# Kernel optimization log

Measured on AMD Instinct MI355X. Metric: run time of the kernel, lower is better.

## Reference

```python
import jax, jax.numpy as jnp
import numpy as np

DIM = 2048
ORDER = 1
# upper-triangular index pairs (i<j), row-major over i then j — matches torch loop order
_IU_ROWS, _IU_COLS = np.triu_indices(DIM, k=1)


def setup_inputs() -> dict:
    key = jax.random.key(0)
    k1, k2 = jax.random.split(key)
    num_params = DIM * (DIM - 1) // 2
    x = jax.random.normal(k1, (4, 4096, DIM), dtype=jnp.float32)
    angles = jax.random.normal(k2, (num_params,), dtype=jnp.float32) * 0.01
    bias = jnp.zeros((DIM,), dtype=jnp.float32)
    return {"x": x, "angles": angles, "bias": bias}


def _skew_symmetric(angles):
    # A[i,j] = angles[k], A[j,i] = -angles[k] for upper-tri (i<j)
    A = jnp.zeros((DIM, DIM), dtype=angles.dtype)
    A = A.at[_IU_ROWS, _IU_COLS].set(angles)
    return A - A.T


def _cayley_approx(A, order=ORDER):
    # W = (I + A + ... + A^order) @ (I + A)
    I = jnp.eye(DIM, dtype=A.dtype)
    inv_approx = I
    A_power = A
    for _ in range(order):
        inv_approx = inv_approx + A_power
        A_power = A_power @ A
    return inv_approx @ (I + A)


def reference(x, angles, bias):
    A = _skew_symmetric(angles)
    W = _cayley_approx(A)
    # [b, s, d] @ [d, d] -> [b, s, d]
    out = jnp.einsum('bsd,de->bse', x, W) + bias
    return out
```

## Files before the change

### kernel.cpp

```cpp
#include <hip/hip_runtime.h>
#include <stdint.h>

#define DIM 2048

typedef short short8 __attribute__((ext_vector_type(8)));
typedef float f32x4 __attribute__((ext_vector_type(4)));

__device__ __forceinline__ unsigned short f2bf(float f) {
    union { float f; unsigned int u; } v;
    v.f = f;
    unsigned int r = v.u + 0x7FFFu + ((v.u >> 16) & 1u);
    return (unsigned short)(r >> 16);
}
__device__ __forceinline__ float bf2f(unsigned short u) {
    union { unsigned int u; float f; } v;
    v.u = ((unsigned int)u) << 16;
    return v.f;
}

__device__ __forceinline__ void async16(const unsigned short* g, unsigned short* l) {
    __builtin_amdgcn_global_load_lds(
        (__attribute__((address_space(1))) void*)(uintptr_t)g,
        (__attribute__((address_space(3))) void*)(uintptr_t)l,
        16, 0, 0);
}

__global__ __launch_bounds__(256) void build_A_tiled(const float* __restrict__ ang,
                                                     unsigned short* __restrict__ A) {
    __shared__ float tile[64][65];
    int b = blockIdx.x;
    int ti = 0, rem = b;
    while (rem >= 32 - ti) { rem -= 32 - ti; ++ti; }
    const int tj = ti + rem;
    const int t  = threadIdx.x;
    const int lj = t & 63;
    const int lw = t >> 6;
    const bool diag = (ti == tj);

#pragma unroll
    for (int m = 0; m < 16; ++m) {
        const int li = lw * 16 + m;
        const int i = ti * 64 + li;
        const int j = tj * 64 + lj;
        float v = 0.0f;
        if (i < j) v = ang[i * (4095 - i) / 2 + (j - i - 1)];
        tile[li][lj] = v;
    }
    __syncthreads();

#pragma unroll
    for (int m = 0; m < 16; ++m) {
        const int li = lw * 16 + m;
        float v;
        if (diag) {
            if (li < lj)      v =  tile[li][lj];
            else if (li > lj) v = -tile[lj][li];
            else              v = 0.0f;
        } else {
            v = tile[li][lj];
        }
        A[(size_t)(ti * 64 + li) * DIM + tj * 64 + lj] = f2bf(v);
    }
    if (!diag) {
#pragma unroll
        for (int m = 0; m < 16; ++m) {
            const int li = lw * 16 + m;
            A[(size_t)(tj * 64 + li) * DIM + ti * 64 + lj] = f2bf(-tile[lj][li]);
        }
    }
}

__global__ __launch_bounds__(256) void s64sym_cvt(
        const unsigned short* __restrict__ A,
        unsigned short* __restrict__ Wt,
        const float* __restrict__ x,
        unsigned short* __restrict__ xbf) {
    __shared__ __align__(16) unsigned short smem[12288];
    unsigned short* ldsA = smem;
    unsigned short* ldsB = smem + 4096;
    float* ldsT = (float*)smem;

    if (blockIdx.x >= 528) {
        const int i = ((blockIdx.x - 528) * 256 + threadIdx.x) * 8;
        const float4 v0 = *(const float4*)(x + i);
        const float4 v1 = *(const float4*)(x + i + 4);
        unsigned short o[8];
        o[0] = f2bf(v0.x); o[1] = f2bf(v0.y); o[2] = f2bf(v0.z); o[3] = f2bf(v0.w);
        o[4] = f2bf(v1.x); o[5] = f2bf(v1.y); o[6] = f2bf(v1.z); o[7] = f2bf(v1.w);
        *(short8*)(xbf + i) = *(short8*)(o);
        return;
    }

    const int K = DIM, N = DIM;
    const int t = threadIdx.x;
    const int swz = (blockIdx.x & 7) * 66 + (blockIdx.x >> 3);
    int ti = 0, rem = swz;
    while (rem >= 32 - ti) { rem -= 32 - ti; ++ti; }
    const int tj = ti + rem;
    const int bm = ti * 64;
    const int bn = tj * 64;

    const int lane = t & 63;
    const int wave = t >> 6;
    const int waveM = (wave >> 1) * 32;
    const int waveN = (wave & 1) * 32;
    const int fm = lane & 15;
    const int fq = lane >> 4;

    f32x4 acc[2][2];
#pragma unroll
    for (int i = 0; i < 2; ++i)
#pragma unroll
        for (int j = 0; j < 2; ++j)
            acc[i][j] = (f32x4){0.f, 0.f, 0.f, 0.f};

    const int trow   = t >> 3;
    const int tchunk = (t & 7) ^ (trow & 7);
    const unsigned short* gA = A + (size_t)(bm + trow) * K + tchunk * 8;
    const unsigned short* gB = A + (size_t)(bn + trow) * K + tchunk * 8;
    const size_t rowskip = (size_t)32 * K;
    unsigned short* lA = ldsA + t * 8;
    unsigned short* lB = ldsB + t * 8;

    for (int kt = 0; kt < K; kt += 64) {
        __syncthreads();
        async16(gA + kt, lA);
        async16(gA + kt + rowskip, lA + 2048);
        async16(gB + kt, lB);
        async16(gB + kt + rowskip, lB + 2048);
        __syncthreads();

#pragma unroll
        for (int ks = 0; ks < 2; ++ks) {
            short8 af[2], bfv[2];
#pragma unroll
            for (int i = 0; i < 2; ++i) {
                const int rowA = waveM + i * 16 + fm;
                const int rowB = waveN + i * 16 + fm;
                af[i]  = *(const short8*)(ldsA + rowA * 64 + (((ks << 2) + fq) ^ (rowA & 7)) * 8);
                bfv[i] = *(const short8*)(ldsB + rowB * 64 + (((ks << 2) + fq) ^ (rowB & 7)) * 8);
            }
#pragma unroll
            for (int i = 0; i < 2; ++i)
#pragma unroll
                for (int j = 0; j < 2; ++j)
                    acc[i][j] = __builtin_amdgcn_mfma_f32_16x16x32_bf16(
                        af[i], bfv[j], acc[i][j], 0, 0, 0);
        }
    }

    __syncthreads();
#pragma unroll
    for (int i = 0; i < 2; ++i) {
#pragma unroll
        for (int j = 0; j < 2; ++j) {
            const int lj = waveN + j * 16 + fm;
            const int gj = bn + lj;
#pragma unroll
            for (int r = 0; r < 4; ++r) {
                const int li = waveM + i * 16 + fq * 4 + r;
                const int gi = bm + li;
                const float a = bf2f(A[(size_t)gi * N + gj]);
                const float s = acc[i][j][r];
                const float d = (gi == gj) ? 1.0f : 0.0f;
                Wt[(size_t)gi * N + gj] = f2bf(d - 2.0f * a - s);
                ldsT[lj * 65 + li] = d + 2.0f * a - s;
            }
        }
    }
    __syncthreads();
    {
        const int r  = t >> 2;
        const int cb = (t & 3) * 16;
        unsigned short o[16];
#pragma unroll
        for (int u = 0; u < 16; ++u)
            o[u] = f2bf(ldsT[r * 65 + cb + u]);
        *(short8*)(Wt + (size_t)(bn + r) * N + bm + cb)     = *(short8*)(o);
        *(short8*)(Wt + (size_t)(bn + r) * N + bm + cb + 8) = *(short8*)(o + 8);
    }
}


#define WAITV(N) asm volatile("s_waitcnt vmcnt(" #N ")" ::: "memory")
#define BAR() do { asm volatile("" ::: "memory"); __builtin_amdgcn_s_barrier(); asm volatile("" ::: "memory"); } while (0)

#define STG_A(BUF, R0, KT) async16(gA + (size_t)(R0) * 2048 + (KT), &ldsA[BUF][(R0) * 64 + t * 8])
#define STG_B(BUF, R0, KT) async16(gB + (size_t)(R0) * 2048 + (KT), &ldsB[BUF][(R0) * 64 + t * 8])

#define READ_A_(BUF, IH) do { \
    _Pragma("unroll") \
    for (int ii = 0; ii < 4; ++ii) { \
        const int row  = waveM + (IH) * 64 + ii * 16 + fm; \
        const int base = row * 64; \
        af[ii][0] = *(const short8*)(&ldsA[BUF][base + ((fq    ) ^ (row & 7)) * 8]); \
        af[ii][1] = *(const short8*)(&ldsA[BUF][base + ((fq + 4) ^ (row & 7)) * 8]); \
    } } while (0)

#define READ_B_(BUF, JH) do { \
    _Pragma("unroll") \
    for (int jj = 0; jj < 2; ++jj) { \
        const int row  = (JH) * 128 + wn * 32 + jj * 16 + fm; \
        const int base = row * 64; \
        bfr[JH][jj][0] = *(const short8*)(&ldsB[BUF][base + ((fq    ) ^ (row & 7)) * 8]); \
        bfr[JH][jj][1] = *(const short8*)(&ldsB[BUF][base + ((fq + 4) ^ (row & 7)) * 8]); \
    } } while (0)

#define MMAQ(IH, JH) do { \
    __builtin_amdgcn_s_setprio(1); \
    _Pragma("unroll") \
    for (int ks = 0; ks < 2; ++ks) \
    _Pragma("unroll") \
    for (int ii = 0; ii < 4; ++ii) \
    _Pragma("unroll") \
    for (int jj = 0; jj < 2; ++jj) \
        acc[(IH) * 4 + ii][(JH) * 2 + jj] = __builtin_amdgcn_mfma_f32_16x16x32_bf16( \
            af[ii][ks], bfr[JH][jj][ks], acc[(IH) * 4 + ii][(JH) * 2 + jj], 0, 0, 0); \
    __builtin_amdgcn_s_setprio(0); \
} while (0)

#define TILE(BUF, KTN, PRE, VN, NXT) do { \
     \
    BAR(); \
    if (PRE) { STG_A(BUF, 0, KTN); STG_A(BUF, 128, KTN); STG_B(BUF, 0, KTN); STG_B(BUF, 64, KTN); } \
    MMAQ(0, 0); \
    READ_B_(BUF, 1); \
     \
    BAR(); \
    if (PRE) { STG_B(BUF, 128, KTN); STG_B(BUF, 192, KTN); } \
    MMAQ(0, 1); \
    READ_A_(BUF, 1); \
     \
    WAITV(VN); \
    BAR(); \
    if (PRE) { STG_A(BUF, 64, KTN); STG_A(BUF, 192, KTN); } \
    MMAQ(1, 0); \
    if (NXT) READ_B_((BUF) ^ 1, 0); \
     \
    BAR(); \
    MMAQ(1, 1); \
    if (NXT) READ_A_((BUF) ^ 1, 0); \
} while (0)

#define TILE_LAST(BUF) do { \
    BAR(); MMAQ(0, 0); READ_B_(BUF, 1); \
    BAR(); MMAQ(0, 1); READ_A_(BUF, 1); \
    BAR(); MMAQ(1, 0); \
    MMAQ(1, 1); \
} while (0)

__global__ __launch_bounds__(512, 2) void gemm_main(
        const unsigned short* __restrict__ Aop,
        const unsigned short* __restrict__ Bop,
        int M, int N, int K,
        const float* __restrict__ bias,
        float* __restrict__ out) {
    __shared__ __align__(16) unsigned short ldsA[2][256 * 64];
    __shared__ __align__(16) unsigned short ldsB[2][256 * 64];

    const int t    = threadIdx.x;
    const int flat = blockIdx.y * 8 + blockIdx.x;
    const int swz  = (flat & 7) * 64 + (flat >> 3);
    const int bn   = (swz & 7) * 256;
    const int bm   = (swz >> 3) * 256;
    const int lane = t & 63;
    const int wave = t >> 6;
    const int wm   = wave >> 2;
    const int wn   = wave & 3;
    const int waveM = wm * 128;
    const int fm = lane & 15;
    const int fq = lane >> 4;

    f32x4 acc[8][4];
#pragma unroll
    for (int i = 0; i < 8; ++i)
#pragma unroll
        for (int j = 0; j < 4; ++j)
            acc[i][j] = (f32x4){0.f, 0.f, 0.f, 0.f};

    short8 af[4][2];
    short8 bfr[2][2][2];

    const int trow   = t >> 3;
    const int tchunk = (t & 7) ^ (trow & 7);
    const unsigned short* gA = Aop + (size_t)(bm + trow) * 2048 + tchunk * 8;
    const unsigned short* gB = Bop + (size_t)(bn + trow) * 2048 + tchunk * 8;

    STG_A(0, 0, 0);   STG_A(0, 128, 0);  STG_B(0, 0, 0);   STG_B(0, 64, 0);
    STG_B(0, 128, 0); STG_B(0, 192, 0);  STG_A(0, 64, 0);  STG_A(0, 192, 0);
    STG_A(1, 0, 64);  STG_A(1, 128, 64); STG_B(1, 0, 64);  STG_B(1, 64, 64);
    STG_B(1, 128, 64);STG_B(1, 192, 64); STG_A(1, 64, 64); STG_A(1, 192, 64);
    WAITV(8);
    BAR();
    READ_A_(0, 0);
    READ_B_(0, 0);

#pragma unroll 1
    for (int it = 0; it < 15; ++it) {
        const int kt = it * 128;
        TILE(0, kt + 128, 1, 6, 1);
        TILE(1, kt + 192, 1, 6, 1);
    }
    TILE(0, 0, 0, 0, 1);
    TILE_LAST(1);

#pragma unroll
    for (int i = 0; i < 8; ++i) {
        const int row0 = bm + waveM + i * 16 + fq * 4;
#pragma unroll
        for (int j = 0; j < 4; ++j) {
            const int col = bn + (j >> 1) * 128 + wn * 32 + (j & 1) * 16 + fm;
            const float b = bias[col];
#pragma unroll
            for (int r = 0; r < 4; ++r)
                out[(size_t)(row0 + r) * 2048 + col] = acc[i][j][r] + b;
        }
    }
}

extern "C" void kernel_launch(void* const* d_in, const int* in_sizes, int n_in,
                              void* d_out, int out_size, void* d_ws, size_t ws_size,
                              hipStream_t stream) {
    const float* x      = (const float*)d_in[0];
    const float* angles = (const float*)d_in[1];
    const float* bias   = (const float*)d_in[2];
    float* out = (float*)d_out;

    char* ws = (char*)d_ws;
    unsigned short* Abf = (unsigned short*)ws;
    unsigned short* Wt  = (unsigned short*)(ws + (8u << 20));
    unsigned short* xbf = (unsigned short*)(ws + (16u << 20));

    const int M = 4 * 4096;

    build_A_tiled<<<528, 256, 0, stream>>>(angles, Abf);

    s64sym_cvt<<<528 + 16384, 256, 0, stream>>>(Abf, Wt, x, xbf);

    gemm_main<<<dim3(DIM / 256, M / 256), 512, 0, stream>>>(
        xbf, Wt, M, DIM, DIM, bias, out);
}
```

Baseline: 349.9 us.

## Double-buffer async loads in symmetric A^2 kernel and reorder main GEMM LDS reads

Replaces the single-buffered load-then-compute loop in the A@A kernel with a two-stage LDS ping-pong. Each iteration prefetches tile k+2 while the MFMAs for the current tile run, and vmcnt waits replace the full syncs. LDS use grows from 24KB to 32KB per block. The main GEMM also issues the B-half LDS reads before the first MFMA quadrant instead of after. This adds ordering risk around reuse of the buffers.

```diff
diff --git a/kernel.cpp b/kernel.cpp
--- a/kernel.cpp
+++ b/kernel.cpp
@@ -24,6 +24,9 @@
         (__attribute__((address_space(3))) void*)(uintptr_t)l,
         16, 0, 0);
 }
+
+#define WAITV(N) asm volatile("s_waitcnt vmcnt(" #N ")" ::: "memory")
+#define BAR() do { asm volatile("" ::: "memory"); __builtin_amdgcn_s_barrier(); asm volatile("" ::: "memory"); } while (0)
 
 __global__ __launch_bounds__(256) void build_A_tiled(const float* __restrict__ ang,
                                                      unsigned short* __restrict__ A) {
@@ -70,14 +73,48 @@
     }
 }
 
+#define S64_ITER(LA, LB, TI, PRE, VN) do { \
+    WAITV(VN); \
+    BAR(); \
+    short8 saf[2][2], sbf[2][2]; \
+    _Pragma("unroll") \
+    for (int ks = 0; ks < 2; ++ks) \
+    _Pragma("unroll") \
+    for (int i = 0; i < 2; ++i) { \
+        const int rowA = waveM + i * 16 + fm; \
+        const int rowB = waveN + i * 16 + fm; \
+        saf[i][ks] = *(const short8*)((LA) + rowA * 64 + (((ks << 2) + fq) ^ (rowA & 7)) * 8); \
+        sbf[i][ks] = *(const short8*)((LB) + rowB * 64 + (((ks << 2) + fq) ^ (rowB & 7)) * 8); \
+    } \
+    asm volatile("s_waitcnt lgkmcnt(0)" ::: "memory"); \
+    __builtin_amdgcn_sched_barrier(0); \
+    BAR(); \
+    if (PRE) { \
+        async16(gA + ((TI) + 2) * 64,           (LA) + t * 8); \
+        async16(gA + ((TI) + 2) * 64 + rowskip, (LA) + 2048 + t * 8); \
+        async16(gB + ((TI) + 2) * 64,           (LB) + t * 8); \
+        async16(gB + ((TI) + 2) * 64 + rowskip, (LB) + 2048 + t * 8); \
+    } \
+    _Pragma("unroll") \
+    for (int ks = 0; ks < 2; ++ks) \
+    _Pragma("unroll") \
+    for (int i = 0; i < 2; ++i) \
+    _Pragma("unroll") \
+    for (int j = 0; j < 2; ++j) \
+        acc[i][j] = __builtin_amdgcn_mfma_f32_16x16x32_bf16( \
+            saf[i][ks], sbf[j][ks], acc[i][j], 0, 0, 0); \
+} while (0)
+
 __global__ __launch_bounds__(256) void s64sym_cvt(
         const unsigned short* __restrict__ A,
         unsigned short* __restrict__ Wt,
         const float* __restrict__ x,
         unsigned short* __restrict__ xbf) {
-    __shared__ __align__(16) unsigned short smem[12288];
-    unsigned short* ldsA = smem;
-    unsigned short* ldsB = smem + 4096;
+    __shared__ __align__(16) unsigned short smem[16384];
+    unsigned short* ldsA0 = smem;
+    unsigned short* ldsA1 = smem + 4096;
+    unsigned short* ldsB0 = smem + 8192;
+    unsigned short* ldsB1 = smem + 12288;
     float* ldsT = (float*)smem;
 
     if (blockIdx.x >= 528) {
@@ -119,35 +156,23 @@
     const unsigned short* gA = A + (size_t)(bm + trow) * K + tchunk * 8;
     const unsigned short* gB = A + (size_t)(bn + trow) * K + tchunk * 8;
     const size_t rowskip = (size_t)32 * K;
-    unsigned short* lA = ldsA + t * 8;
-    unsigned short* lB = ldsB + t * 8;
-
-    for (int kt = 0; kt < K; kt += 64) {
-        __syncthreads();
-        async16(gA + kt, lA);
-        async16(gA + kt + rowskip, lA + 2048);
-        async16(gB + kt, lB);
-        async16(gB + kt + rowskip, lB + 2048);
-        __syncthreads();
-
-#pragma unroll
-        for (int ks = 0; ks < 2; ++ks) {
-            short8 af[2], bfv[2];
-#pragma unroll
-            for (int i = 0; i < 2; ++i) {
-                const int rowA = waveM + i * 16 + fm;
-                const int rowB = waveN + i * 16 + fm;
-                af[i]  = *(const short8*)(ldsA + rowA * 64 + (((ks << 2) + fq) ^ (rowA & 7)) * 8);
-                bfv[i] = *(const short8*)(ldsB + rowB * 64 + (((ks << 2) + fq) ^ (rowB & 7)) * 8);
-            }
-#pragma unroll
-            for (int i = 0; i < 2; ++i)
-#pragma unroll
-                for (int j = 0; j < 2; ++j)
-                    acc[i][j] = __builtin_amdgcn_mfma_f32_16x16x32_bf16(
-                        af[i], bfv[j], acc[i][j], 0, 0, 0);
-        }
-    }
+
+    async16(gA,            ldsA0 + t * 8);
+    async16(gA + rowskip,  ldsA0 + 2048 + t * 8);
+    async16(gB,            ldsB0 + t * 8);
+    async16(gB + rowskip,  ldsB0 + 2048 + t * 8);
+    async16(gA + 64,           ldsA1 + t * 8);
+    async16(gA + 64 + rowskip, ldsA1 + 2048 + t * 8);
+    async16(gB + 64,           ldsB1 + t * 8);
+    async16(gB + 64 + rowskip, ldsB1 + 2048 + t * 8);
+
+#pragma unroll 1
+    for (int ii = 0; ii < 15; ++ii) {
+        S64_ITER(ldsA0, ldsB0, ii * 2,     1, 4);
+        S64_ITER(ldsA1, ldsB1, ii * 2 + 1, 1, 4);
+    }
+    S64_ITER(ldsA0, ldsB0, 30, 0, 4);
+    S64_ITER(ldsA1, ldsB1, 31, 0, 0);
 
     __syncthreads();
 #pragma unroll
@@ -182,9 +207,6 @@
 }
 
 
-#define WAITV(N) asm volatile("s_waitcnt vmcnt(" #N ")" ::: "memory")
-#define BAR() do { asm volatile("" ::: "memory"); __builtin_amdgcn_s_barrier(); asm volatile("" ::: "memory"); } while (0)
-
 #define STG_A(BUF, R0, KT) async16(gA + (size_t)(R0) * 2048 + (KT), &ldsA[BUF][(R0) * 64 + t * 8])
 #define STG_B(BUF, R0, KT) async16(gB + (size_t)(R0) * 2048 + (KT), &ldsB[BUF][(R0) * 64 + t * 8])
 
@@ -223,8 +245,8 @@
      \
     BAR(); \
     if (PRE) { STG_A(BUF, 0, KTN); STG_A(BUF, 128, KTN); STG_B(BUF, 0, KTN); STG_B(BUF, 64, KTN); } \
+    READ_B_(BUF, 1); \
     MMAQ(0, 0); \
-    READ_B_(BUF, 1); \
      \
     BAR(); \
     if (PRE) { STG_B(BUF, 128, KTN); STG_B(BUF, 192, KTN); } \
@@ -243,7 +265,7 @@
 } while (0)
 
 #define TILE_LAST(BUF) do { \
-    BAR(); MMAQ(0, 0); READ_B_(BUF, 1); \
+    BAR(); READ_B_(BUF, 1); MMAQ(0, 0); \
     BAR(); MMAQ(0, 1); READ_A_(BUF, 1); \
     BAR(); MMAQ(1, 0); \
     MMAQ(1, 1); \
```

Measured after the change: 359.5 us. +2.7%, slower.
